# Optimization experiments

Hardware: AMD Instinct MI355X
Metric: run time of the kernel (lower is better)

Reference implementation:

```python
import jax, jax.numpy as jnp
import numpy as np
from functools import partial

NUM_ITERS = 3
NUM_CAPS = 8      # primary capsule count
NUM_CLASSES = 10
OUT_CH = 16       # digit capsule dim
INPUT_SIZE = 32 * 6 * 6  # 1152 primary capsule units per capsule map


def squash(s, axis=-1):
    # faithful to non_linear_squashing: s * (||s||^2/(1+||s||^2)) / (||s||+1e-10)
    norm_sqr = jnp.sum(s * s, axis=axis, keepdims=True)
    scale = jnp.sqrt(norm_sqr) + 1e-10
    mag = norm_sqr / (1.0 + norm_sqr)
    return s * mag / scale


def conv2d(x, w, b, stride):
    y = jax.lax.conv_general_dilated(
        x, w, window_strides=(stride, stride), padding='VALID',
        dimension_numbers=('NCHW', 'OIHW', 'NCHW'))
    return y + b[None, :, None, None]


def setup_inputs() -> dict:
    key = jax.random.key(0)
    ks = jax.random.split(key, 6)
    B = 256
    x = jax.random.normal(ks[0], (B, 1, 28, 28), dtype=jnp.float32)
    conv_w = jax.random.normal(ks[1], (256, 1, 9, 9), dtype=jnp.float32) * 0.05
    conv_b = jax.random.normal(ks[2], (256,), dtype=jnp.float32) * 0.05
    # 8 primary capsule conv units (256->32 each) fused into one 256->256 conv
    prim_w = jax.random.normal(ks[3], (NUM_CAPS * 32, 256, 9, 9), dtype=jnp.float32) * 0.02
    prim_b = jax.random.normal(ks[4], (NUM_CAPS * 32,), dtype=jnp.float32) * 0.02
    # digit routing weights (input_size, num_classes, out_channels, num_capsules)
    digit_w = jax.random.normal(ks[5], (INPUT_SIZE, NUM_CLASSES, OUT_CH, NUM_CAPS), dtype=jnp.float32)
    return {'x': x, 'conv_w': conv_w, 'conv_b': conv_b,
            'prim_w': prim_w, 'prim_b': prim_b, 'digit_w': digit_w}


def reference(x, conv_w, conv_b, prim_w, prim_b, digit_w):
    B = x.shape[0]
    # conv stack: 1->256 k9 s1 + ReLU  (28 -> 20); pool is MaxPool2d(1,1) = identity
    h = jax.nn.relu(conv2d(x, conv_w, conv_b, stride=1))  # (B,256,20,20)
    # primary capsules: 8 convs 256->32 k9 s2, no activation (nl_activation=False)
    p = conv2d(h, prim_w, prim_b, stride=2)               # (B,256,6,6)
    u = p.reshape(B, NUM_CAPS, -1)                        # (B,8,1152)
    u = squash(u, axis=-1)
    # digit layer with dynamic routing
    # u_i: (B, IS, 8);  u_j_i[b,i,c,o] = sum_k W[i,c,o,k] * u_i[b,i,k]
    u_i = jnp.transpose(u, (0, 2, 1))                     # (B,1152,8)
    u_j_i = jnp.einsum('icok,bik->bico', digit_w, u_i)    # (B,1152,10,16)
    b_ij = jnp.zeros((INPUT_SIZE, NUM_CLASSES), dtype=x.dtype)
    out = None
    for _ in range(NUM_ITERS):
        c_ij = jax.nn.softmax(b_ij, axis=0)               # softmax over input capsules (dim=1 in torch)
        s_j = jnp.einsum('ic,bico->bco', c_ij, u_j_i)     # (B,10,16)
        # original squashes (B,1,C,16,1) along dim=2 == the CLASS axis
        out = squash(s_j, axis=1)                         # (B,10,16)
        # agreement: mean over batch of <u_j_i, v_j>
        u_v = jnp.einsum('bico,bco->ic', u_j_i, out) / B  # (1152,10)
        b_ij = b_ij + u_v
    # torch returns out.squeeze(1) with shape (B, C, 16, 1)
    return out[..., None]
```

## Files before the change

kernel.cpp:

```cpp
#include <hip/hip_runtime.h>
#include <cstdint>
#include <cstddef>


typedef __attribute__((ext_vector_type(8))) short short8;
typedef __attribute__((ext_vector_type(4))) float f32x4;

#define PHALF 2359296

__device__ __forceinline__ unsigned short f2bf_rn(float x) {
    unsigned u = __float_as_uint(x);
    unsigned r = (u + 0x7fffu + ((u >> 16) & 1u)) >> 16;
    return (unsigned short)r;
}

__global__ void k_makew(const float* __restrict__ w2,
                        unsigned short* __restrict__ wt) {
    __shared__ float lw[20736];
    int ocg = blockIdx.x, icg = blockIdx.y, t = threadIdx.x;
    for (int idx = t; idx < 20736; idx += 256) {
        int row = idx / 81, k = idx % 81;
        int oc_l = row >> 5, ic_l = row & 31;
        lw[idx] = w2[((size_t)(ocg * 8 + oc_l) * 256 + icg * 32 + ic_l) * 81 + k];
    }
    __syncthreads();
    for (int idx = t; idx < 2592; idx += 256) {
        int k = idx >> 5;
        int r = idx & 31;
        int oc_l = r >> 2, sl = r & 3;
        unsigned short hi8[8];
        #pragma unroll
        for (int j = 0; j < 8; j++)
            hi8[j] = f2bf_rn(lw[(oc_l * 32 + sl * 8 + j) * 81 + k]);
        size_t o = ((size_t)(k * 256 + ocg * 8 + oc_l)) * 256 + icg * 32 + sl * 8;
        *(uint4*)&wt[o] = *(uint4*)hi8;
    }
}

__global__ void k_prep2(const float* __restrict__ cw, const float* __restrict__ dw,
                        unsigned short* __restrict__ wb1, float* __restrict__ dwT2,
                        float* __restrict__ bij) {
    int blk = blockIdx.x, t = threadIdx.x;
    if (blk == 0) {
        for (int idx = t; idx < 24576; idx += 256) {
            int j = idx & 7, lane = (idx >> 3) & 63;
            int q = (idx >> 9) % 3, nt = idx / 1536;
            int oc = nt * 16 + (lane & 15);
            int kg = q * 32 + (lane >> 4) * 8 + j;
            float v = (kg < 81) ? cw[oc * 81 + kg] : 0.f;
            wb1[idx] = f2bf_rn(v);
        }
    } else if (blk == 1) {
        for (int idx = t; idx < 11520; idx += 256) bij[idx] = 0.f;
    } else {
        int co = blk - 2;
        int c = co >> 4, o = co & 15;
        const float* base = dw + c * 128 + o * 8;
        float* out = dwT2 + (size_t)co * 9216;
        for (int idx = t; idx < 9216; idx += 256) {
            int i = idx >> 3, k = idx & 7;
            out[idx] = base[(size_t)i * 1280 + k];
        }
    }
}

__global__ __launch_bounds__(256) void k_conv1m(
    const float* __restrict__ x, const unsigned short* __restrict__ wb1,
    const float* __restrict__ cb, unsigned short* __restrict__ h)
{
    __shared__ unsigned short xb[900];
    int b = blockIdx.x, ng = blockIdx.y, t = threadIdx.x;
    int w = t >> 6, l = t & 63;
    for (int idx = t; idx < 900; idx += 256) {
        int row = idx / 30, col = idx % 30;
        float v = (row < 28 && col < 28) ? x[(size_t)b * 784 + row * 28 + col] : 0.f;
        xb[idx] = f2bf_rn(v);
    }
    __syncthreads();
    int lane16 = l & 15, l4 = l >> 4;
    int ntile = (w == 0) ? 7 : 6;
    short8 afr[7][3];
    for (int i = 0; i < 7; i++) {
        if (i < ntile) {
            int mt = w + 4 * i;
            int pix = mt * 16 + lane16;
            int py = pix / 20, px = pix % 20;
            #pragma unroll
            for (int qq = 0; qq < 3; qq++) {
                int kbase = qq * 32 + l4 * 8;
                unsigned short tmp[8];
                int ky = kbase / 9, kx = kbase - 9 * (kbase / 9);
                #pragma unroll
                for (int j = 0; j < 8; j++) {
                    tmp[j] = xb[(py + ky) * 30 + px + kx];
                    kx++; if (kx == 9) { kx = 0; ky++; }
                }
                afr[i][qq] = *(short8*)tmp;
            }
        }
    }
    for (int nt0 = 0; nt0 < 8; nt0++) {
        int nt = ng * 8 + nt0;
        short8 bfr[3];
        #pragma unroll
        for (int qq = 0; qq < 3; qq++)
            bfr[qq] = *(const short8*)&wb1[(nt * 3 + qq) * 512 + l * 8];
        float bias = cb[nt * 16 + lane16];
        f32x4 acc[7] = {};
        for (int i = 0; i < 7; i++) {
            if (i < ntile) {
                #pragma unroll
                for (int qq = 0; qq < 3; qq++)
                    acc[i] = __builtin_amdgcn_mfma_f32_16x16x32_bf16(afr[i][qq], bfr[qq], acc[i], 0, 0, 0);
            }
        }
        for (int i = 0; i < 7; i++) {
            if (i < ntile) {
                int mt = w + 4 * i;
                int pixb = mt * 16 + l4 * 4;
                size_t base = ((size_t)b * 400 + pixb) * 256 + nt * 16 + lane16;
                #pragma unroll
                for (int r = 0; r < 4; r++) {
                    float v = fmaxf(acc[i][r] + bias, 0.f);
                    h[base + (size_t)r * 256] = f2bf_rn(v);
                }
            }
        }
    }
}

__global__ __launch_bounds__(256) void k_conv2m(
    const unsigned short* __restrict__ h,
    const unsigned short* __restrict__ wt,
    float* __restrict__ pp)
{
    __shared__ unsigned short smem[12288];
    const int t = threadIdx.x;
    const int w = t >> 6, l = t & 63;
    const int mb = blockIdx.x, nb = blockIdx.y, z = blockIdx.z;

    const unsigned short* src;
    int nld, sbase;
    unsigned rowbase[8];
    if (w < 2) {
        src = h; nld = 8; sbase = w * 4096;
        #pragma unroll
        for (int ld = 0; ld < 8; ld++) {
            int row = w * 64 + ld * 8 + (l >> 3);
            int c = l & 7;
            int g = c ^ (row & 7);
            int P = mb * 128 + row;
            int b = P / 36, o = P % 36;
            int oy = o / 6, ox = o % 6;
            rowbase[ld] = (unsigned)((b * 400 + oy * 40 + ox * 2) * 256 + z * 64 + g * 8);
        }
    } else {
        int hh = w - 2;
        src = wt; nld = 4; sbase = 8192 + hh * 2048;
        #pragma unroll
        for (int ld = 0; ld < 4; ld++) {
            int oc = hh * 32 + ld * 8 + (l >> 3);
            int c = l & 7;
            int g = c ^ (oc & 7);
            rowbase[ld] = (unsigned)((nb * 64 + oc) * 256 + z * 64 + g * 8);
        }
    }

    const int wm = w & 1, wn = w >> 1;
    const int lane16 = l & 15, q = l >> 4;

    f32x4 acc[4][2] = {};

    for (int ky = 0; ky < 9; ky++) {
        for (int kx = 0; kx < 9; kx++) {
            const unsigned kofs = (w < 2) ? (unsigned)((ky * 20 + kx) * 256)
                                          : (unsigned)((ky * 9 + kx) * 65536);
            __syncthreads();
            for (int ld = 0; ld < nld; ld++) {
                __builtin_amdgcn_global_load_lds(
                    (const __attribute__((address_space(1))) unsigned int*)(const void*)(src + rowbase[ld] + kofs),
                    (__attribute__((address_space(3))) unsigned int*)(void*)(smem + sbase + ld * 512),
                    16, 0, 0);
            }
            __syncthreads();
            #pragma unroll
            for (int ic2 = 0; ic2 < 2; ic2++) {
                short8 a[4], b[2];
                #pragma unroll
                for (int mt = 0; mt < 4; mt++) {
                    int pixL = wm * 64 + mt * 16 + lane16;
                    int ps = (ic2 * 4 + q) ^ (pixL & 7);
                    a[mt] = *(const short8*)(smem + pixL * 64 + ps * 8);
                }
                #pragma unroll
                for (int nt = 0; nt < 2; nt++) {
                    int ocL = wn * 32 + nt * 16 + lane16;
                    int ps = (ic2 * 4 + q) ^ (ocL & 7);
                    b[nt] = *(const short8*)(smem + 8192 + ocL * 64 + ps * 8);
                }
                #pragma unroll
                for (int mt = 0; mt < 4; mt++)
                    #pragma unroll
                    for (int nt = 0; nt < 2; nt++)
                        acc[mt][nt] = __builtin_amdgcn_mfma_f32_16x16x32_bf16(a[mt], b[nt], acc[mt][nt], 0, 0, 0);
            }
        }
    }

    float* pout = pp + (size_t)z * PHALF;
    #pragma unroll
    for (int mt = 0; mt < 4; mt++) {
        int pixG = mb * 128 + wm * 64 + mt * 16 + q * 4;
        int b = pixG / 36, p36 = pixG % 36;
        #pragma unroll
        for (int nt = 0; nt < 2; nt++) {
            int oc = nb * 64 + wn * 32 + nt * 16 + lane16;
            f32x4 v = acc[mt][nt];
            *(f32x4*)&pout[((size_t)(b * 256 + oc)) * 36 + p36] = v;
        }
    }
}

__global__ void k_squash1(const float* __restrict__ pp, const float* __restrict__ prim_b,
                          float* __restrict__ U, float* __restrict__ UT) {
    __shared__ float red[4];
    int b = blockIdx.x >> 3, cap = blockIdx.x & 7;
    int t = threadIdx.x;
    const float* pa = pp + ((size_t)b * 256 + cap * 32) * 36;
    float v[5];
    float ss = 0.f;
    #pragma unroll
    for (int j = 0; j < 5; j++) {
        int idx = t + j * 256;
        if (idx < 1152) {
            int ch_l = idx / 36;
            float val = pa[idx] + pa[idx + PHALF] + pa[idx + 2 * PHALF] +
                        pa[idx + 3 * PHALF] + prim_b[cap * 32 + ch_l];
            v[j] = val; ss += val * val;
        } else v[j] = 0.f;
    }
    for (int off = 32; off; off >>= 1) ss += __shfl_down(ss, off);
    if ((t & 63) == 0) red[t >> 6] = ss;
    __syncthreads();
    float n2 = red[0] + red[1] + red[2] + red[3];
    float f = (n2 / (1.0f + n2)) / (sqrtf(n2) + 1e-10f);
    #pragma unroll
    for (int j = 0; j < 5; j++) {
        int idx = t + j * 256;
        if (idx < 1152) {
            float r = v[j] * f;
            U[(size_t)b * 9216 + idx * 8 + cap] = r;
            UT[(size_t)(idx * 8 + cap) * 256 + b] = r;
        }
    }
}

__global__ void k_softmax(const float* __restrict__ bij, float* __restrict__ csm) {
    __shared__ float red[4];
    int c = blockIdx.x, t = threadIdx.x;
    float vals[5];
    float mx = -1e30f;
    #pragma unroll
    for (int j = 0; j < 5; j++) {
        int i = t + j * 256;
        vals[j] = (i < 1152) ? bij[i * 10 + c] : -1e30f;
        mx = fmaxf(mx, vals[j]);
    }
    for (int off = 32; off; off >>= 1) mx = fmaxf(mx, __shfl_down(mx, off));
    if ((t & 63) == 0) red[t >> 6] = mx;
    __syncthreads();
    mx = fmaxf(fmaxf(red[0], red[1]), fmaxf(red[2], red[3]));
    __syncthreads();
    float s = 0.f;
    #pragma unroll
    for (int j = 0; j < 5; j++) {
        int i = t + j * 256;
        vals[j] = (i < 1152) ? expf(vals[j] - mx) : 0.f;
        s += vals[j];
    }
    for (int off = 32; off; off >>= 1) s += __shfl_down(s, off);
    if ((t & 63) == 0) red[t >> 6] = s;
    __syncthreads();
    s = red[0] + red[1] + red[2] + red[3];
    float inv = 1.0f / s;
    #pragma unroll
    for (int j = 0; j < 5; j++) {
        int i = t + j * 256;
        if (i < 1152) csm[i * 10 + c] = vals[j] * inv;
    }
}

__global__ __launch_bounds__(256) void k_gemm1(const float* __restrict__ U,
                                               const float* __restrict__ dwT2,
                                               const float* __restrict__ csm,
                                               float* __restrict__ part,
                                               int uniform) {
    __shared__ float Us[32 * 36];
    __shared__ float WsT[5120];
    __shared__ float cl[360];
    int mb = blockIdx.x, kc = blockIdx.y, t = threadIdx.x;
    int tc = t & 15, tb = t >> 4;
    if (!uniform)
        for (int idx = t; idx < 360; idx += 256) cl[idx] = csm[kc * 360 + idx];
    const float uscale = 1.0f / 1152.0f;
    float acc[2][10] = {};
    for (int ks = 0; ks < 9; ks++) {
        __syncthreads();
        {
            int bb = t >> 3, k4 = t & 7;
            *(float4*)&Us[bb * 36 + k4 * 4] =
                *(const float4*)&U[(size_t)(mb * 32 + bb) * 9216 + kc * 288 + ks * 32 + k4 * 4];
        }
        #pragma unroll
        for (int pass = 0; pass < 5; pass++) {
            int s = t + pass * 256;
            int co = s >> 3, p = s & 7;
            int kq = p ^ (co & 7);
            int ikl = ks * 32 + kq * 4;
            float4 v = *(const float4*)&dwT2[(size_t)co * 9216 + kc * 288 + ikl];
            float sc = uniform ? uscale : cl[(ikl >> 3) * 10 + (co >> 4)];
            v.x *= sc; v.y *= sc; v.z *= sc; v.w *= sc;
            *(float4*)&WsT[s * 4] = v;
        }
        __syncthreads();
        float a0[32], a1[32];
        #pragma unroll
        for (int kq = 0; kq < 8; kq++) {
            float4 v0 = *(const float4*)&Us[(tb * 2) * 36 + kq * 4];
            float4 v1 = *(const float4*)&Us[(tb * 2 + 1) * 36 + kq * 4];
            a0[kq * 4 + 0] = v0.x; a0[kq * 4 + 1] = v0.y; a0[kq * 4 + 2] = v0.z; a0[kq * 4 + 3] = v0.w;
            a1[kq * 4 + 0] = v1.x; a1[kq * 4 + 1] = v1.y; a1[kq * 4 + 2] = v1.z; a1[kq * 4 + 3] = v1.w;
        }
        #pragma unroll
        for (int j = 0; j < 10; j++) {
            int co = tc + 16 * j;
            int cx = co & 7, cbase = co * 32;
            #pragma unroll
            for (int kq = 0; kq < 8; kq++) {
                float4 wv = *(const float4*)&WsT[cbase + ((kq ^ cx) << 2)];
                acc[0][j] += a0[kq * 4 + 0] * wv.x; acc[0][j] += a0[kq * 4 + 1] * wv.y;
                acc[0][j] += a0[kq * 4 + 2] * wv.z; acc[0][j] += a0[kq * 4 + 3] * wv.w;
                acc[1][j] += a1[kq * 4 + 0] * wv.x; acc[1][j] += a1[kq * 4 + 1] * wv.y;
                acc[1][j] += a1[kq * 4 + 2] * wv.z; acc[1][j] += a1[kq * 4 + 3] * wv.w;
            }
        }
    }
    #pragma unroll
    for (int r = 0; r < 2; r++)
        #pragma unroll
        for (int j = 0; j < 10; j++)
            part[(size_t)kc * 40960 + (mb * 32 + tb * 2 + r) * 160 + tc + 16 * j] = acc[r][j];
}

__global__ void k_redsq(const float* __restrict__ part, float* __restrict__ out,
                        float* __restrict__ outT, int writeT) {
    __shared__ float sl[160];
    __shared__ float n2s[16];
    int b = blockIdx.x, t = threadIdx.x;
    float s = 0.f;
    if (t < 160) {
        for (int kc = 0; kc < 32; kc++) s += part[(size_t)kc * 40960 + b * 160 + t];
        sl[t] = s;
    }
    __syncthreads();
    if (t < 16) {
        float n2 = 0.f;
        #pragma unroll
        for (int c = 0; c < 10; c++) { float v = sl[c * 16 + t]; n2 += v * v; }
        n2s[t] = n2;
    }
    __syncthreads();
    if (t < 160) {
        float n2 = n2s[t & 15];
        float f = (n2 / (1.0f + n2)) / (sqrtf(n2) + 1e-10f);
        float r = s * f;
        out[(size_t)b * 160 + t] = r;
        if (writeT) outT[(size_t)t * 256 + b] = r;
    }
}

__global__ __launch_bounds__(256) void k_g2uv(const float* __restrict__ UT,
                                              const float* __restrict__ outTg,
                                              const float* __restrict__ dw,
                                              float* __restrict__ bij) {
    __shared__ float UsT[1024];
    __shared__ float OsT[5120];
    __shared__ float dwl[5120];
    __shared__ float sb[320];
    int blk = blockIdx.x, t = threadIdx.x;
    int tc = t & 15, tm = t >> 4;
    for (int idx = t; idx < 5120; idx += 256)
        dwl[idx] = dw[(size_t)blk * 5120 + idx];
    float acc[2][10] = {};
    for (int bs = 0; bs < 256; bs += 32) {
        __syncthreads();
        {
            int m = t >> 3, p = t & 7;
            int kq = p ^ (m & 7);
            *(float4*)&UsT[t * 4] =
                *(const float4*)&UT[(size_t)(blk * 32 + m) * 256 + bs + kq * 4];
        }
        #pragma unroll
        for (int pass = 0; pass < 5; pass++) {
            int s = t + pass * 256;
            int co = s >> 3, p = s & 7;
            int kq = p ^ (co & 7);
            *(float4*)&OsT[s * 4] =
                *(const float4*)&outTg[(size_t)co * 256 + bs + kq * 4];
        }
        __syncthreads();
        float a0[32], a1[32];
        int m0 = tm * 2, m1 = tm * 2 + 1;
        #pragma unroll
        for (int kq = 0; kq < 8; kq++) {
            float4 v0 = *(const float4*)&UsT[m0 * 32 + ((kq ^ (m0 & 7)) << 2)];
            float4 v1 = *(const float4*)&UsT[m1 * 32 + ((kq ^ (m1 & 7)) << 2)];
            a0[kq * 4 + 0] = v0.x; a0[kq * 4 + 1] = v0.y; a0[kq * 4 + 2] = v0.z; a0[kq * 4 + 3] = v0.w;
            a1[kq * 4 + 0] = v1.x; a1[kq * 4 + 1] = v1.y; a1[kq * 4 + 2] = v1.z; a1[kq * 4 + 3] = v1.w;
        }
        #pragma unroll
        for (int j = 0; j < 10; j++) {
            int co = tc + 16 * j;
            int cx = co & 7, cbase = co * 32;
            #pragma unroll
            for (int kq = 0; kq < 8; kq++) {
                float4 wv = *(const float4*)&OsT[cbase + ((kq ^ cx) << 2)];
                acc[0][j] += a0[kq * 4 + 0] * wv.x; acc[0][j] += a0[kq * 4 + 1] * wv.y;
                acc[0][j] += a0[kq * 4 + 2] * wv.z; acc[0][j] += a0[kq * 4 + 3] * wv.w;
                acc[1][j] += a1[kq * 4 + 0] * wv.x; acc[1][j] += a1[kq * 4 + 1] * wv.y;
                acc[1][j] += a1[kq * 4 + 2] * wv.z; acc[1][j] += a1[kq * 4 + 3] * wv.w;
            }
        }
    }
    #pragma unroll
    for (int r = 0; r < 2; r++) {
        int ik_l = tm * 2 + r;
        int i_l = ik_l >> 3, k = ik_l & 7;
        #pragma unroll
        for (int j = 0; j < 10; j++) {
            float v = acc[r][j] * dwl[i_l * 1280 + (j * 16 + tc) * 8 + k];
            v += __shfl_down(v, 8, 16);
            v += __shfl_down(v, 4, 16);
            v += __shfl_down(v, 2, 16);
            v += __shfl_down(v, 1, 16);
            if (tc == 0) sb[ik_l * 10 + j] = v;
        }
    }
    __syncthreads();
    if (t < 40) {
        int i_l = t / 10, c = t % 10;
        float s = 0.f;
        #pragma unroll
        for (int kk = 0; kk < 8; kk++) s += sb[(i_l * 8 + kk) * 10 + c];
        size_t o = (size_t)(blk * 4 + i_l) * 10 + c;
        bij[o] += s * (1.0f / 256.0f);
    }
}

extern "C" void kernel_launch(void* const* d_in, const int* in_sizes, int n_in,
                              void* d_out, int out_size, void* d_ws, size_t ws_size,
                              hipStream_t stream) {
    const float* x      = (const float*)d_in[0];
    const float* conv_w = (const float*)d_in[1];
    const float* conv_b = (const float*)d_in[2];
    const float* prim_w = (const float*)d_in[3];
    const float* prim_b = (const float*)d_in[4];
    const float* dw     = (const float*)d_in[5];

    char* wsb = (char*)d_ws;
    unsigned short* h   = (unsigned short*)(wsb);
    unsigned short* wt  = (unsigned short*)(wsb + 52428800);
    float* pp   = (float*)(wsb + 63045632);
    float* U    = (float*)(wsb + 100794368);
    float* dwT2 = (float*)(wsb + 110231552);
    float* part = (float*)(wsb + 116129792);
    float* csm  = (float*)(wsb + 121372672);
    float* bij  = (float*)(wsb + 121418752);
    float* outT = (float*)(wsb + 121464832);
    float* outw = (float*)(wsb + 121628672);
    float* UT   = (float*)(wsb + 121792512);
    unsigned short* wb1 = (unsigned short*)(wsb + 131229696);

    k_makew<<<dim3(32, 8), 256, 0, stream>>>(prim_w, wt);
    k_prep2<<<162, 256, 0, stream>>>(conv_w, dw, wb1, dwT2, bij);
    k_conv1m<<<dim3(256, 2), 256, 0, stream>>>(x, wb1, conv_b, h);
    k_conv2m<<<dim3(72, 4, 4), 256, 0, stream>>>(h, wt, pp);
    k_squash1<<<2048, 256, 0, stream>>>(pp, prim_b, U, UT);

    k_gemm1<<<dim3(8, 32), 256, 0, stream>>>(U, dwT2, csm, part, 1);
    k_redsq<<<256, 256, 0, stream>>>(part, outw, outT, 1);
    k_g2uv<<<288, 256, 0, stream>>>(UT, outT, dw, bij);
    k_softmax<<<10, 256, 0, stream>>>(bij, csm);
    k_gemm1<<<dim3(8, 32), 256, 0, stream>>>(U, dwT2, csm, part, 0);
    k_redsq<<<256, 256, 0, stream>>>(part, outw, outT, 1);
    k_g2uv<<<288, 256, 0, stream>>>(UT, outT, dw, bij);
    k_softmax<<<10, 256, 0, stream>>>(bij, csm);
    k_gemm1<<<dim3(8, 32), 256, 0, stream>>>(U, dwT2, csm, part, 0);
    k_redsq<<<256, 256, 0, stream>>>(part, (float*)d_out, outT, 0);
}
```

Before: 532.3 us.

## Load conv2 MFMA fragments directly from global, halve split-K, separate UT transpose

The primary-capsule conv kernel drops its LDS staging and barriers and reads bf16 A/B fragments straight from global memory into MFMA operands. It splits the input-channel reduction into 2 slices instead of 4, so each block does twice the K work and squash sums two partials instead of four. The strided UT scatter in squash moves into a separate tiled-transpose kernel. b_ij zeroing is replaced by an init flag in the first agreement pass, and the unused redsq output buffer is removed. Direct global fragment loads lose LDS reuse and depend on L1/L2 hits for the shared pixel and weight rows.

```diff
diff --git a/kernel.cpp b/kernel.cpp
--- a/kernel.cpp
+++ b/kernel.cpp
@@ -38,8 +38,7 @@
 }
 
 __global__ void k_prep2(const float* __restrict__ cw, const float* __restrict__ dw,
-                        unsigned short* __restrict__ wb1, float* __restrict__ dwT2,
-                        float* __restrict__ bij) {
+                        unsigned short* __restrict__ wb1, float* __restrict__ dwT2) {
     int blk = blockIdx.x, t = threadIdx.x;
     if (blk == 0) {
         for (int idx = t; idx < 24576; idx += 256) {
@@ -50,10 +49,8 @@
             float v = (kg < 81) ? cw[oc * 81 + kg] : 0.f;
             wb1[idx] = f2bf_rn(v);
         }
-    } else if (blk == 1) {
-        for (int idx = t; idx < 11520; idx += 256) bij[idx] = 0.f;
     } else {
-        int co = blk - 2;
+        int co = blk - 1;
         int c = co >> 4, o = co & 15;
         const float* base = dw + c * 128 + o * 8;
         float* out = dwT2 + (size_t)co * 9216;
@@ -129,80 +126,56 @@
     }
 }
 
-__global__ __launch_bounds__(256) void k_conv2m(
+__global__ __launch_bounds__(256) void k_conv2d(
     const unsigned short* __restrict__ h,
     const unsigned short* __restrict__ wt,
     float* __restrict__ pp)
 {
-    __shared__ unsigned short smem[12288];
     const int t = threadIdx.x;
     const int w = t >> 6, l = t & 63;
     const int mb = blockIdx.x, nb = blockIdx.y, z = blockIdx.z;
-
-    const unsigned short* src;
-    int nld, sbase;
-    unsigned rowbase[8];
-    if (w < 2) {
-        src = h; nld = 8; sbase = w * 4096;
-        #pragma unroll
-        for (int ld = 0; ld < 8; ld++) {
-            int row = w * 64 + ld * 8 + (l >> 3);
-            int c = l & 7;
-            int g = c ^ (row & 7);
-            int P = mb * 128 + row;
-            int b = P / 36, o = P % 36;
-            int oy = o / 6, ox = o % 6;
-            rowbase[ld] = (unsigned)((b * 400 + oy * 40 + ox * 2) * 256 + z * 64 + g * 8);
-        }
-    } else {
-        int hh = w - 2;
-        src = wt; nld = 4; sbase = 8192 + hh * 2048;
-        #pragma unroll
-        for (int ld = 0; ld < 4; ld++) {
-            int oc = hh * 32 + ld * 8 + (l >> 3);
-            int c = l & 7;
-            int g = c ^ (oc & 7);
-            rowbase[ld] = (unsigned)((nb * 64 + oc) * 256 + z * 64 + g * 8);
-        }
-    }
-
     const int wm = w & 1, wn = w >> 1;
     const int lane16 = l & 15, q = l >> 4;
 
+    const unsigned short* abase[4];
+    #pragma unroll
+    for (int mt = 0; mt < 4; mt++) {
+        int P = mb * 128 + wm * 64 + mt * 16 + lane16;
+        int b = P / 36, o = P % 36;
+        int oy = o / 6, ox = o % 6;
+        abase[mt] = h + ((size_t)(b * 400 + oy * 40 + ox * 2) * 256 + z * 128 + q * 8);
+    }
+    const unsigned short* bbase[2];
+    #pragma unroll
+    for (int nt = 0; nt < 2; nt++) {
+        int oc = nb * 64 + wn * 32 + nt * 16 + lane16;
+        bbase[nt] = wt + ((size_t)oc * 256 + z * 128 + q * 8);
+    }
+
     f32x4 acc[4][2] = {};
 
     for (int ky = 0; ky < 9; ky++) {
         for (int kx = 0; kx < 9; kx++) {
-            const unsigned kofs = (w < 2) ? (unsigned)((ky * 20 + kx) * 256)
-                                          : (unsigned)((ky * 9 + kx) * 65536);
-            __syncthreads();
-            for (int ld = 0; ld < nld; ld++) {
-                __builtin_amdgcn_global_load_lds(
-                    (const __attribute__((address_space(1))) unsigned int*)(const void*)(src + rowbase[ld] + kofs),
-                    (__attribute__((address_space(3))) unsigned int*)(void*)(smem + sbase + ld * 512),
-                    16, 0, 0);
-            }
-            __syncthreads();
+            const unsigned aofs = (unsigned)((ky * 20 + kx) * 256);
+            const size_t bofs = (size_t)(ky * 9 + kx) * 65536;
             #pragma unroll
-            for (int ic2 = 0; ic2 < 2; ic2++) {
-                short8 a[4], b[2];
+            for (int hh = 0; hh < 2; hh++) {
                 #pragma unroll
-                for (int mt = 0; mt < 4; mt++) {
-                    int pixL = wm * 64 + mt * 16 + lane16;
-                    int ps = (ic2 * 4 + q) ^ (pixL & 7);
-                    a[mt] = *(const short8*)(smem + pixL * 64 + ps * 8);
-                }
-                #pragma unroll
-                for (int nt = 0; nt < 2; nt++) {
-                    int ocL = wn * 32 + nt * 16 + lane16;
-                    int ps = (ic2 * 4 + q) ^ (ocL & 7);
-                    b[nt] = *(const short8*)(smem + 8192 + ocL * 64 + ps * 8);
-                }
-                #pragma unroll
-                for (int mt = 0; mt < 4; mt++)
+                for (int ic2 = 0; ic2 < 2; ic2++) {
+                    const unsigned sub = hh * 64 + ic2 * 32;
+                    short8 a[4], b[2];
+                    #pragma unroll
+                    for (int mt = 0; mt < 4; mt++)
+                        a[mt] = *(const short8*)(abase[mt] + aofs + sub);
                     #pragma unroll
                     for (int nt = 0; nt < 2; nt++)
-                        acc[mt][nt] = __builtin_amdgcn_mfma_f32_16x16x32_bf16(a[mt], b[nt], acc[mt][nt], 0, 0, 0);
+                        b[nt] = *(const short8*)(bbase[nt] + bofs + sub);
+                    #pragma unroll
+                    for (int mt = 0; mt < 4; mt++)
+                        #pragma unroll
+                        for (int nt = 0; nt < 2; nt++)
+                            acc[mt][nt] = __builtin_amdgcn_mfma_f32_16x16x32_bf16(a[mt], b[nt], acc[mt][nt], 0, 0, 0);
+                }
             }
         }
     }
@@ -222,11 +195,12 @@
 }
 
 __global__ void k_squash1(const float* __restrict__ pp, const float* __restrict__ prim_b,
-                          float* __restrict__ U, float* __restrict__ UT) {
+                          float* __restrict__ U) {
     __shared__ float red[4];
     int b = blockIdx.x >> 3, cap = blockIdx.x & 7;
     int t = threadIdx.x;
     const float* pa = pp + ((size_t)b * 256 + cap * 32) * 36;
+    const float* pc = pa + PHALF;
     float v[5];
     float ss = 0.f;
     #pragma unroll
@@ -234,8 +208,7 @@
         int idx = t + j * 256;
         if (idx < 1152) {
             int ch_l = idx / 36;
-            float val = pa[idx] + pa[idx + PHALF] + pa[idx + 2 * PHALF] +
-                        pa[idx + 3 * PHALF] + prim_b[cap * 32 + ch_l];
+            float val = pa[idx] + pc[idx] + prim_b[cap * 32 + ch_l];
             v[j] = val; ss += val * val;
         } else v[j] = 0.f;
     }
@@ -247,11 +220,27 @@
     #pragma unroll
     for (int j = 0; j < 5; j++) {
         int idx = t + j * 256;
-        if (idx < 1152) {
-            float r = v[j] * f;
-            U[(size_t)b * 9216 + idx * 8 + cap] = r;
-            UT[(size_t)(idx * 8 + cap) * 256 + b] = r;
-        }
+        if (idx < 1152) U[(size_t)b * 9216 + idx * 8 + cap] = v[j] * f;
+    }
+}
+
+__global__ void k_ut(const float* __restrict__ U, float* __restrict__ UT) {
+    __shared__ float tl[64][65];
+    int ikb = blockIdx.x, bb = blockIdx.y, t = threadIdx.x;
+    for (int idx = t; idx < 1024; idx += 256) {
+        int row = idx >> 4, c4 = idx & 15;
+        float4 v = *(const float4*)&U[(size_t)(bb * 64 + row) * 9216 + ikb * 64 + c4 * 4];
+        tl[c4 * 4 + 0][row] = v.x;
+        tl[c4 * 4 + 1][row] = v.y;
+        tl[c4 * 4 + 2][row] = v.z;
+        tl[c4 * 4 + 3][row] = v.w;
+    }
+    __syncthreads();
+    for (int idx = t; idx < 1024; idx += 256) {
+        int row = idx >> 4, c4 = idx & 15;
+        float4 v = make_float4(tl[row][c4 * 4 + 0], tl[row][c4 * 4 + 1],
+                               tl[row][c4 * 4 + 2], tl[row][c4 * 4 + 3]);
+        *(float4*)&UT[(size_t)(ikb * 64 + row) * 256 + bb * 64 + c4 * 4] = v;
     }
 }
 
@@ -352,8 +341,8 @@
             part[(size_t)kc * 40960 + (mb * 32 + tb * 2 + r) * 160 + tc + 16 * j] = acc[r][j];
 }
 
-__global__ void k_redsq(const float* __restrict__ part, float* __restrict__ out,
-                        float* __restrict__ outT, int writeT) {
+__global__ void k_redsq(const float* __restrict__ part, float* __restrict__ outT,
+                        float* __restrict__ dout, int last) {
     __shared__ float sl[160];
     __shared__ float n2s[16];
     int b = blockIdx.x, t = threadIdx.x;
@@ -374,15 +363,15 @@
         float n2 = n2s[t & 15];
         float f = (n2 / (1.0f + n2)) / (sqrtf(n2) + 1e-10f);
         float r = s * f;
-        out[(size_t)b * 160 + t] = r;
-        if (writeT) outT[(size_t)t * 256 + b] = r;
+        if (last) dout[(size_t)b * 160 + t] = r;
+        else      outT[(size_t)t * 256 + b] = r;
     }
 }
 
 __global__ __launch_bounds__(256) void k_g2uv(const float* __restrict__ UT,
                                               const float* __restrict__ outTg,
                                               const float* __restrict__ dw,
-                                              float* __restrict__ bij) {
+                                              float* __restrict__ bij, int init) {
     __shared__ float UsT[1024];
     __shared__ float OsT[5120];
     __shared__ float dwl[5120];
@@ -453,7 +442,9 @@
         #pragma unroll
         for (int kk = 0; kk < 8; kk++) s += sb[(i_l * 8 + kk) * 10 + c];
         size_t o = (size_t)(blk * 4 + i_l) * 10 + c;
-        bij[o] += s * (1.0f / 256.0f);
+        float val = s * (1.0f / 256.0f);
+        if (init) bij[o] = val;
+        else      bij[o] += val;
     }
 }
 
@@ -471,30 +462,31 @@
     unsigned short* h   = (unsigned short*)(wsb);
     unsigned short* wt  = (unsigned short*)(wsb + 52428800);
     float* pp   = (float*)(wsb + 63045632);
-    float* U    = (float*)(wsb + 100794368);
-    float* dwT2 = (float*)(wsb + 110231552);
-    float* part = (float*)(wsb + 116129792);
-    float* csm  = (float*)(wsb + 121372672);
-    float* bij  = (float*)(wsb + 121418752);
-    float* outT = (float*)(wsb + 121464832);
-    float* outw = (float*)(wsb + 121628672);
-    float* UT   = (float*)(wsb + 121792512);
-    unsigned short* wb1 = (unsigned short*)(wsb + 131229696);
+    float* U    = (float*)(wsb + 81920000);
+    float* dwT2 = (float*)(wsb + 91357184);
+    float* part = (float*)(wsb + 97255424);
+    float* csm  = (float*)(wsb + 102498304);
+    float* bij  = (float*)(wsb + 102544384);
+    float* outT = (float*)(wsb + 102590464);
+    float* UT   = (float*)(wsb + 102754304);
+    unsigned short* wb1 = (unsigned short*)(wsb + 112191488);
+    float* dout = (float*)d_out;
 
     k_makew<<<dim3(32, 8), 256, 0, stream>>>(prim_w, wt);
-    k_prep2<<<162, 256, 0, stream>>>(conv_w, dw, wb1, dwT2, bij);
+    k_prep2<<<161, 256, 0, stream>>>(conv_w, dw, wb1, dwT2);
     k_conv1m<<<dim3(256, 2), 256, 0, stream>>>(x, wb1, conv_b, h);
-    k_conv2m<<<dim3(72, 4, 4), 256, 0, stream>>>(h, wt, pp);
-    k_squash1<<<2048, 256, 0, stream>>>(pp, prim_b, U, UT);
+    k_conv2d<<<dim3(72, 4, 2), 256, 0, stream>>>(h, wt, pp);
+    k_squash1<<<2048, 256, 0, stream>>>(pp, prim_b, U);
+    k_ut<<<dim3(144, 4), 256, 0, stream>>>(U, UT);
 
     k_gemm1<<<dim3(8, 32), 256, 0, stream>>>(U, dwT2, csm, part, 1);
-    k_redsq<<<256, 256, 0, stream>>>(part, outw, outT, 1);
-    k_g2uv<<<288, 256, 0, stream>>>(UT, outT, dw, bij);
+    k_redsq<<<256, 256, 0, stream>>>(part, outT, dout, 0);
+    k_g2uv<<<288, 256, 0, stream>>>(UT, outT, dw, bij, 1);
     k_softmax<<<10, 256, 0, stream>>>(bij, csm);
     k_gemm1<<<dim3(8, 32), 256, 0, stream>>>(U, dwT2, csm, part, 0);
-    k_redsq<<<256, 256, 0, stream>>>(part, outw, outT, 1);
-    k_g2uv<<<288, 256, 0, stream>>>(UT, outT, dw, bij);
+    k_redsq<<<256, 256, 0, stream>>>(part, outT, dout, 0);
+    k_g2uv<<<288, 256, 0, stream>>>(UT, outT, dw, bij, 0);
     k_softmax<<<10, 256, 0, stream>>>(bij, csm);
     k_gemm1<<<dim3(8, 32), 256, 0, stream>>>(U, dwT2, csm, part, 0);
-    k_redsq<<<256, 256, 0, stream>>>(part, (float*)d_out, outT, 0);
-}
+    k_redsq<<<256, 256, 0, stream>>>(part, outT, dout, 1);
+}
```

New measurement: 1.007 ms. 1.89x slower.
